# Performance work log

Hardware: AMD Instinct MI355X
Metric: run time of the kernel (lower is better)

## Reference

```python
import jax, jax.numpy as jnp
import numpy as np

TIMESTEPS = 1000
DIFFUSION_SPEED = 0.01
B, N = 4, 2048
E = N * (N - 1) // 2  # strict lower-triangular entries per graph


def _build_Qt():
    # Qt[t-1] = [[1-f, f], [f, 1-f]],  f = 0.5*(1-(1-2s)^t), t = 1..T
    ts = jnp.arange(1, TIMESTEPS + 1, dtype=jnp.float32)
    flip = 0.5 * (1.0 - (1.0 - 2.0 * DIFFUSION_SPEED) ** ts)          # [T]
    row0 = jnp.stack([1.0 - flip, flip], axis=-1)                      # [T,2]
    row1 = jnp.stack([flip, 1.0 - flip], axis=-1)                      # [T,2]
    return jnp.stack([row0, row1], axis=1)                             # [T,2,2]


def setup_inputs() -> dict:
    key = jax.random.key(0)
    k1, k2, k3, k4 = jax.random.split(key, 4)
    adj_start = jax.random.randint(k1, (B, N, N), 0, 2, dtype=jnp.int32)
    t = jax.random.randint(k2, (B,), 0, TIMESTEPS, dtype=jnp.int32)
    u = jax.random.uniform(k3, (B, N, N), dtype=jnp.float32)
    q_approx = jax.random.normal(k4, (B, E), dtype=jnp.float32)
    return {"adj_start": adj_start, "t": t, "u": u, "q_approx": q_approx}


def reference(adj_start, t, u, q_approx):
    Qt = _build_Qt()                                                   # [T,2,2]
    # symmetrize raw adjacency into a binary undirected adjacency
    a = jnp.tril(adj_start, -1)
    adj0 = a + jnp.swapaxes(a, -1, -2)                                 # [B,N,N] in {0,1}

    b_idx = jnp.arange(B)[:, None, None]

    # ---- forward diffusion: sample x_t ~ Categorical(Qt[t][adj0]) ----
    probs = Qt[t][b_idx, adj0]                                         # [B,N,N,2]
    x_t = (u < probs[..., 1]).astype(adj0.dtype)                       # [B,N,N]

    # ---- backward diffusion: q(x_{t-1} | x_t, x_0) ----
    Q_likelihood = Qt[0]                                               # [2,2]
    Q_prior = Qt[t - 1]                                                # [B,2,2] (t=0 wraps, as in torch)
    Q_evidence = Qt[t]                                                 # [B,2,2]

    likelihood = Q_likelihood[x_t]                                     # [B,N,N,2]
    prior = Q_prior[b_idx, adj0]                                       # [B,N,N,2]
    evidence = Q_evidence[b_idx, adj0, x_t]                            # [B,N,N]
    q_backward = likelihood * prior / evidence[..., None]              # [B,N,N,2]

    ti, tj = np.tril_indices(N, -1)                                    # static indices
    q_target = q_backward[:, ti, tj, 1]                                # [B,E]

    # ---- BCE-with-logits loss (mean) ----
    x = q_approx
    loss = jnp.mean(jnp.maximum(x, 0.0) - x * q_target + jnp.log1p(jnp.exp(-jnp.abs(x))))
    return loss
```

## Files before the change

kernel.cpp:

```cpp
#include <hip/hip_runtime.h>
#include <math.h>

#define TIMESTEPS 1000
constexpr int Bc = 4;
constexpr int Nc = 2048;
constexpr int EcI = Nc * (Nc - 1) / 2;
constexpr int EG  = EcI / 4;

constexpr int BLOCKS_PER_B = 512;
constexpr int THREADS      = 256;
constexpr int GSTRIDE      = BLOCKS_PER_B * THREADS;

typedef int   i4v __attribute__((ext_vector_type(4)));
typedef float f4v __attribute__((ext_vector_type(4)));

__device__ __forceinline__ i4v load_i4u(const int* p) {
    i4v r; __builtin_memcpy(&r, p, 16); return r;
}
__device__ __forceinline__ f4v load_f4u(const float* p) {
    f4v r; __builtin_memcpy(&r, p, 16); return r;
}

__global__ __launch_bounds__(256) void diff_loss_kernel(
    const int* __restrict__ adj, const int* __restrict__ t,
    const float* __restrict__ u, const float* __restrict__ q,
    double* __restrict__ partials)
{
    const int b  = blockIdx.x >> 9;
    const int lb = blockIdx.x & (BLOCKS_PER_B - 1);
    const int tb = t[b];

    const float f_t   = 0.5f * (1.0f - powf(0.98f, (float)(tb + 1)));
    const int   tpe   = (tb == 0) ? TIMESTEPS : tb;
    const float f_p   = 0.5f * (1.0f - powf(0.98f, (float)tpe));
    const float f0    = 0.5f * (1.0f - 0.98f);
    const float omf_t = 1.0f - f_t;

    const float p0   = f_t;
    const float p1   = omf_t;
    const float qt00 = f0          * f_p          / omf_t;
    const float qt01 = (1.0f - f0) * f_p          / f_t;
    const float qt10 = f0          * (1.0f - f_p) / f_t;
    const float qt11 = (1.0f - f0) * (1.0f - f_p) / omf_t;

    const int*   adjb = adj + ((size_t)b << 22);
    const float* ub   = u   + ((size_t)b << 22);
    const float* qb   = q   + (size_t)b * EcI;

    double acc = 0.0;
    int g = lb * THREADS + threadIdx.x;

    #pragma unroll 2
    for (int it = 0; it < 4; ++it, g += GSTRIDE) {
        if (g < EG) {
            const int e0 = g << 2;

            const float sf = sqrtf((float)(8 * e0 + 1));
            int i = (int)((1.0f + sf) * 0.5f);
            if (i * (i - 1) / 2 > e0)  --i;
            if (i * (i + 1) / 2 <= e0) ++i;
            const int j = e0 - i * (i - 1) / 2;

            const f4v q4 = *(const f4v*)(qb + e0);
            float s = 0.0f;

            if (j + 4 <= i) {
                const int base = (i << 11) + j;
                const i4v av = load_i4u(adjb + base);
                const f4v uv = load_f4u(ub   + base);
                #pragma unroll
                for (int k = 0; k < 4; ++k) {
                    const int   a0 = av[k];
                    const float ps = a0 ? p1 : p0;
                    const bool  x  = (uv[k] < ps);
                    const float t0 = x ? qt01 : qt00;
                    const float t1 = x ? qt11 : qt10;
                    const float qtv = a0 ? t1 : t0;
                    const float qv  = q4[k];
                    s += fmaxf(qv, 0.0f) - qv * qtv
                       + __logf(1.0f + __expf(-fabsf(qv)));
                }
            } else {
                int ii = i, jj = j;
                #pragma unroll
                for (int k = 0; k < 4; ++k) {
                    const bool adv = (jj >= ii);
                    ii += adv;
                    jj = adv ? 0 : jj;
                    const int base = (ii << 11) + jj;
                    const int   a0 = adjb[base];
                    const float uu = ub[base];
                    const float ps = a0 ? p1 : p0;
                    const bool  x  = (uu < ps);
                    const float t0 = x ? qt01 : qt00;
                    const float t1 = x ? qt11 : qt10;
                    const float qtv = a0 ? t1 : t0;
                    const float qv  = q4[k];
                    s += fmaxf(qv, 0.0f) - qv * qtv
                       + __logf(1.0f + __expf(-fabsf(qv)));
                    ++jj;
                }
            }
            acc += (double)s;
        }
    }

    for (int off = 32; off > 0; off >>= 1)
        acc += __shfl_down(acc, off, 64);
    __shared__ double wsum[4];
    const int lane = threadIdx.x & 63, wid = threadIdx.x >> 6;
    if (lane == 0) wsum[wid] = acc;
    __syncthreads();
    if (threadIdx.x == 0)
        partials[blockIdx.x] = wsum[0] + wsum[1] + wsum[2] + wsum[3];
}

__global__ __launch_bounds__(256) void final_reduce_kernel(
    const double* __restrict__ partials, int nb, float* __restrict__ out)
{
    double acc = 0.0;
    for (int idx = threadIdx.x; idx < nb; idx += blockDim.x)
        acc += partials[idx];
    for (int off = 32; off > 0; off >>= 1)
        acc += __shfl_down(acc, off, 64);
    __shared__ double wsum[4];
    const int lane = threadIdx.x & 63, wid = threadIdx.x >> 6;
    if (lane == 0) wsum[wid] = acc;
    __syncthreads();
    if (threadIdx.x == 0)
        out[0] = (float)((wsum[0] + wsum[1] + wsum[2] + wsum[3]) /
                         ((double)Bc * (double)EcI));
}

extern "C" void kernel_launch(void* const* d_in, const int* in_sizes, int n_in,
                              void* d_out, int out_size, void* d_ws, size_t ws_size,
                              hipStream_t stream) {
    const int*   adj = (const int*)d_in[0];
    const int*   t   = (const int*)d_in[1];
    const float* u   = (const float*)d_in[2];
    const float* q   = (const float*)d_in[3];
    float*  out      = (float*)d_out;
    double* partials = (double*)d_ws;

    const int NB = Bc * BLOCKS_PER_B;
    diff_loss_kernel<<<NB, THREADS, 0, stream>>>(adj, t, u, q, partials);
    final_reduce_kernel<<<1, 256, 0, stream>>>(partials, NB, out);
}
```

Before: 164.5 us.

## Pair complementary triangle rows per block to drop per-element index math

Rows p+1 and 2047-p of the lower triangle are paired so each pair covers a fixed-size span. Each block handles two pairs with aligned 16-byte loads of adj and u, using masked 4-wide groups instead of sqrt-based index recovery and a scalar fallback path. The q loads become scalar and unaligned because row offsets are not multiples of 4, and a single thread handles the leftover group. Launch bounds now also request 8 blocks per multiprocessor.

```diff
diff --git a/kernel.cpp b/kernel.cpp
--- a/kernel.cpp
+++ b/kernel.cpp
@@ -2,38 +2,79 @@
 #include <math.h>
 
 #define TIMESTEPS 1000
-constexpr int Bc = 4;
-constexpr int Nc = 2048;
+constexpr int Bc  = 4;
+constexpr int Nc  = 2048;
 constexpr int EcI = Nc * (Nc - 1) / 2;
-constexpr int EG  = EcI / 4;
-
-constexpr int BLOCKS_PER_B = 512;
-constexpr int THREADS      = 256;
-constexpr int GSTRIDE      = BLOCKS_PER_B * THREADS;
+constexpr int THREADS = 256;
+constexpr int NB  = 2048;
 
 typedef int   i4v __attribute__((ext_vector_type(4)));
 typedef float f4v __attribute__((ext_vector_type(4)));
 
-__device__ __forceinline__ i4v load_i4u(const int* p) {
-    i4v r; __builtin_memcpy(&r, p, 16); return r;
-}
-__device__ __forceinline__ f4v load_f4u(const float* p) {
-    f4v r; __builtin_memcpy(&r, p, 16); return r;
+__device__ __forceinline__ int imin(int a, int b) { return a < b ? a : b; }
+
+struct Grp {
+    i4v av; f4v uv;
+    float q0, q1, q2, q3;
+    int jg, len;
+};
+
+__device__ __forceinline__ Grp load_group(
+    const int* __restrict__ adjb, const float* __restrict__ ub,
+    const float* __restrict__ qb, int gg, int la, int lb, int rb, int Ga)
+{
+    Grp g;
+    const bool ina = gg < Ga;
+    const int row  = ina ? la : rb;
+    g.len = ina ? la : lb;
+    g.jg  = (ina ? gg : (gg - Ga)) << 2;
+    const int base = (row << 11) + g.jg;
+    g.av = *(const i4v*)(adjb + base);
+    g.uv = *(const f4v*)(ub + base);
+    const int tri = (row * (row - 1)) >> 1;
+    const int e   = tri + g.jg;
+    g.q0 = qb[imin(e,     EcI - 1)];
+    g.q1 = qb[imin(e + 1, EcI - 1)];
+    g.q2 = qb[imin(e + 2, EcI - 1)];
+    g.q3 = qb[imin(e + 3, EcI - 1)];
+    return g;
 }
 
-__global__ __launch_bounds__(256) void diff_loss_kernel(
+__device__ __forceinline__ float grp_term(const Grp& g,
+    float p0, float p1, float qt00, float qt01, float qt10, float qt11)
+{
+    const float qs[4] = {g.q0, g.q1, g.q2, g.q3};
+    float s = 0.0f;
+    #pragma unroll
+    for (int k = 0; k < 4; ++k) {
+        const int   a0 = g.av[k];
+        const float ps = a0 ? p1 : p0;
+        const bool  x  = g.uv[k] < ps;
+        const float t0 = x ? qt01 : qt00;
+        const float t1 = x ? qt11 : qt10;
+        const float qt = a0 ? t1 : t0;
+        const float qv = qs[k];
+        const float term = fmaxf(qv, 0.0f) - qv * qt
+                         + __logf(1.0f + __expf(-fabsf(qv)));
+        s += (g.jg + k < g.len) ? term : 0.0f;
+    }
+    return s;
+}
+
+__global__ __launch_bounds__(256, 8) void diff_loss_kernel(
     const int* __restrict__ adj, const int* __restrict__ t,
     const float* __restrict__ u, const float* __restrict__ q,
     double* __restrict__ partials)
 {
-    const int b  = blockIdx.x >> 9;
-    const int lb = blockIdx.x & (BLOCKS_PER_B - 1);
-    const int tb = t[b];
+    const int blk = blockIdx.x;
+    const int b   = blk >> 9;
+    const int ip  = blk & 511;
+    const int tb  = t[b];
 
     const float f_t   = 0.5f * (1.0f - powf(0.98f, (float)(tb + 1)));
     const int   tpe   = (tb == 0) ? TIMESTEPS : tb;
     const float f_p   = 0.5f * (1.0f - powf(0.98f, (float)tpe));
-    const float f0    = 0.5f * (1.0f - 0.98f);
+    const float f0    = 0.01f;
     const float omf_t = 1.0f - f_t;
 
     const float p0   = f_t;
@@ -47,61 +88,35 @@
     const float* ub   = u   + ((size_t)b << 22);
     const float* qb   = q   + (size_t)b * EcI;
 
+    const int tid = threadIdx.x;
     double acc = 0.0;
-    int g = lb * THREADS + threadIdx.x;
 
-    #pragma unroll 2
-    for (int it = 0; it < 4; ++it, g += GSTRIDE) {
-        if (g < EG) {
-            const int e0 = g << 2;
+    #pragma unroll
+    for (int pp = 0; pp < 2; ++pp) {
+        const int p  = 2 * ip + pp;
+        const int la = p + 1;
+        const int rb = 2047 - p;
+        const int lb = (p == 1023) ? 0 : rb;
+        const int Ga = (la + 3) >> 2;
 
-            const float sf = sqrtf((float)(8 * e0 + 1));
-            int i = (int)((1.0f + sf) * 0.5f);
-            if (i * (i - 1) / 2 > e0)  --i;
-            if (i * (i + 1) / 2 <= e0) ++i;
-            const int j = e0 - i * (i - 1) / 2;
+        Grp g0 = load_group(adjb, ub, qb, tid,       la, lb, rb, Ga);
+        Grp g1 = load_group(adjb, ub, qb, tid + 256, la, lb, rb, Ga);
+        acc += (double)grp_term(g0, p0, p1, qt00, qt01, qt10, qt11);
+        acc += (double)grp_term(g1, p0, p1, qt00, qt01, qt10, qt11);
+    }
 
-            const f4v q4 = *(const f4v*)(qb + e0);
-            float s = 0.0f;
-
-            if (j + 4 <= i) {
-                const int base = (i << 11) + j;
-                const i4v av = load_i4u(adjb + base);
-                const f4v uv = load_f4u(ub   + base);
-                #pragma unroll
-                for (int k = 0; k < 4; ++k) {
-                    const int   a0 = av[k];
-                    const float ps = a0 ? p1 : p0;
-                    const bool  x  = (uv[k] < ps);
-                    const float t0 = x ? qt01 : qt00;
-                    const float t1 = x ? qt11 : qt10;
-                    const float qtv = a0 ? t1 : t0;
-                    const float qv  = q4[k];
-                    s += fmaxf(qv, 0.0f) - qv * qtv
-                       + __logf(1.0f + __expf(-fabsf(qv)));
-                }
-            } else {
-                int ii = i, jj = j;
-                #pragma unroll
-                for (int k = 0; k < 4; ++k) {
-                    const bool adv = (jj >= ii);
-                    ii += adv;
-                    jj = adv ? 0 : jj;
-                    const int base = (ii << 11) + jj;
-                    const int   a0 = adjb[base];
-                    const float uu = ub[base];
-                    const float ps = a0 ? p1 : p0;
-                    const bool  x  = (uu < ps);
-                    const float t0 = x ? qt01 : qt00;
-                    const float t1 = x ? qt11 : qt10;
-                    const float qtv = a0 ? t1 : t0;
-                    const float qv  = q4[k];
-                    s += fmaxf(qv, 0.0f) - qv * qtv
-                       + __logf(1.0f + __expf(-fabsf(qv)));
-                    ++jj;
-                }
+    if (tid == 0) {
+        #pragma unroll
+        for (int pp = 0; pp < 2; ++pp) {
+            const int p  = 2 * ip + pp;
+            const int la = p + 1;
+            if (la & 3) {
+                const int rb = 2047 - p;
+                const int lb = (p == 1023) ? 0 : rb;
+                const int Ga = (la + 3) >> 2;
+                Grp gt = load_group(adjb, ub, qb, 512, la, lb, rb, Ga);
+                acc += (double)grp_term(gt, p0, p1, qt00, qt01, qt10, qt11);
             }
-            acc += (double)s;
         }
     }
 
@@ -142,7 +157,6 @@
     float*  out      = (float*)d_out;
     double* partials = (double*)d_ws;
 
-    const int NB = Bc * BLOCKS_PER_B;
     diff_loss_kernel<<<NB, THREADS, 0, stream>>>(adj, t, u, q, partials);
     final_reduce_kernel<<<1, 256, 0, stream>>>(partials, NB, out);
 }
```

Result: no change. 163.3 us (-0.7%).

## Software-pipeline group loads with two-deep prefetch over fewer larger blocks

Applied to the files above, without the earlier changes.

Restructures the main kernel so each thread handles two element groups per iteration, issuing the loads for the groups two iterations ahead while reducing the current ones. The grid shrinks to 128 blocks per graph with a 2D launch, and each thread now covers 16 groups. The vectorized fast path for row-contained groups is dropped in favor of always using scalar per-element gather loads. This aims to hide memory latency via register prefetching, but it raises register pressure and loses the 16-byte vector loads.

```diff
diff --git a/kernel.cpp b/kernel.cpp
--- a/kernel.cpp
+++ b/kernel.cpp
@@ -2,38 +2,80 @@
 #include <math.h>
 
 #define TIMESTEPS 1000
-constexpr int Bc = 4;
-constexpr int Nc = 2048;
+constexpr int Bc  = 4;
+constexpr int Nc  = 2048;
 constexpr int EcI = Nc * (Nc - 1) / 2;
 constexpr int EG  = EcI / 4;
 
-constexpr int BLOCKS_PER_B = 512;
-constexpr int THREADS      = 256;
-constexpr int GSTRIDE      = BLOCKS_PER_B * THREADS;
+constexpr int BLKX    = 128;
+constexpr int THREADS = 256;
+constexpr int ITERS   = 8;
+constexpr int ITERSTRIDE = BLKX * THREADS * 2;
 
 typedef int   i4v __attribute__((ext_vector_type(4)));
 typedef float f4v __attribute__((ext_vector_type(4)));
 
-__device__ __forceinline__ i4v load_i4u(const int* p) {
-    i4v r; __builtin_memcpy(&r, p, 16); return r;
-}
-__device__ __forceinline__ f4v load_f4u(const float* p) {
-    f4v r; __builtin_memcpy(&r, p, 16); return r;
+__device__ __forceinline__ int imin(int a, int b) { return a < b ? a : b; }
+
+struct GData { i4v av; f4v uv; f4v qv; };
+
+__device__ __forceinline__ GData issue_group(
+    const int* __restrict__ adjb, const float* __restrict__ ub,
+    const float* __restrict__ qb, int gc)
+{
+    GData d;
+    const int e0 = gc << 2;
+    const float sf = sqrtf((float)(8 * e0 + 1));
+    int i = (int)((1.0f + sf) * 0.5f);
+    if (i * (i - 1) / 2 > e0)  --i;
+    if (i * (i + 1) / 2 <= e0) ++i;
+    int jj = e0 - i * (i - 1) / 2;
+    d.qv = *(const f4v*)(qb + e0);
+    int ii = i;
+    #pragma unroll
+    for (int k = 0; k < 4; ++k) {
+        const bool adv = (jj >= ii);
+        ii += adv;
+        jj = adv ? 0 : jj;
+        const int base = (ii << 11) + jj;
+        d.av[k] = adjb[base];
+        d.uv[k] = ub[base];
+        ++jj;
+    }
+    return d;
 }
 
-__global__ __launch_bounds__(256) void diff_loss_kernel(
+__device__ __forceinline__ float group_sum(const GData& d,
+    float p0, float p1, float qt00, float qt01, float qt10, float qt11)
+{
+    float s = 0.0f;
+    #pragma unroll
+    for (int k = 0; k < 4; ++k) {
+        const int   a0 = d.av[k];
+        const float ps = a0 ? p1 : p0;
+        const bool  x  = d.uv[k] < ps;
+        const float t0 = x ? qt01 : qt00;
+        const float t1 = x ? qt11 : qt10;
+        const float qt = a0 ? t1 : t0;
+        const float qq = d.qv[k];
+        s += fmaxf(qq, 0.0f) - qq * qt + __logf(1.0f + __expf(-fabsf(qq)));
+    }
+    return s;
+}
+
+__global__ __launch_bounds__(256, 2) void diff_loss_kernel(
     const int* __restrict__ adj, const int* __restrict__ t,
     const float* __restrict__ u, const float* __restrict__ q,
     double* __restrict__ partials)
 {
-    const int b  = blockIdx.x >> 9;
-    const int lb = blockIdx.x & (BLOCKS_PER_B - 1);
+    const int b  = blockIdx.y;
+    const int bx = blockIdx.x;
     const int tb = t[b];
 
     const float f_t   = 0.5f * (1.0f - powf(0.98f, (float)(tb + 1)));
     const int   tpe   = (tb == 0) ? TIMESTEPS : tb;
     const float f_p   = 0.5f * (1.0f - powf(0.98f, (float)tpe));
-    const float f0    = 0.5f * (1.0f - 0.98f);
+    const float f0    = 0.01f;
     const float omf_t = 1.0f - f_t;
 
     const float p0   = f_t;
@@ -47,62 +89,30 @@
     const float* ub   = u   + ((size_t)b << 22);
     const float* qb   = q   + (size_t)b * EcI;
 
+    const int gbase = bx * 512 + threadIdx.x;
+
+    GData A0 = issue_group(adjb, ub, qb, gbase);
+    GData B0 = issue_group(adjb, ub, qb, gbase + 256);
+    GData A1 = issue_group(adjb, ub, qb, gbase + ITERSTRIDE);
+    GData B1 = issue_group(adjb, ub, qb, gbase + ITERSTRIDE + 256);
+
     double acc = 0.0;
-    int g = lb * THREADS + threadIdx.x;
 
-    #pragma unroll 2
-    for (int it = 0; it < 4; ++it, g += GSTRIDE) {
-        if (g < EG) {
-            const int e0 = g << 2;
+    #pragma unroll 1
+    for (int k = 0; k < ITERS; ++k) {
+        GData An = A1, Bn = B1;
+        if (k + 2 < ITERS) {
+            const int gk = gbase + (k + 2) * ITERSTRIDE;
+            An = issue_group(adjb, ub, qb, gk);
+            Bn = issue_group(adjb, ub, qb, imin(gk + 256, EG - 1));
+        }
 
-            const float sf = sqrtf((float)(8 * e0 + 1));
-            int i = (int)((1.0f + sf) * 0.5f);
-            if (i * (i - 1) / 2 > e0)  --i;
-            if (i * (i + 1) / 2 <= e0) ++i;
-            const int j = e0 - i * (i - 1) / 2;
+        const float sA = group_sum(A0, p0, p1, qt00, qt01, qt10, qt11);
+        const float sB = group_sum(B0, p0, p1, qt00, qt01, qt10, qt11);
+        const int g1 = gbase + k * ITERSTRIDE + 256;
+        acc += (double)(sA + ((g1 < EG) ? sB : 0.0f));
 
-            const f4v q4 = *(const f4v*)(qb + e0);
-            float s = 0.0f;
-
-            if (j + 4 <= i) {
-                const int base = (i << 11) + j;
-                const i4v av = load_i4u(adjb + base);
-                const f4v uv = load_f4u(ub   + base);
-                #pragma unroll
-                for (int k = 0; k < 4; ++k) {
-                    const int   a0 = av[k];
-                    const float ps = a0 ? p1 : p0;
-                    const bool  x  = (uv[k] < ps);
-                    const float t0 = x ? qt01 : qt00;
-                    const float t1 = x ? qt11 : qt10;
-                    const float qtv = a0 ? t1 : t0;
-                    const float qv  = q4[k];
-                    s += fmaxf(qv, 0.0f) - qv * qtv
-                       + __logf(1.0f + __expf(-fabsf(qv)));
-                }
-            } else {
-                int ii = i, jj = j;
-                #pragma unroll
-                for (int k = 0; k < 4; ++k) {
-                    const bool adv = (jj >= ii);
-                    ii += adv;
-                    jj = adv ? 0 : jj;
-                    const int base = (ii << 11) + jj;
-                    const int   a0 = adjb[base];
-                    const float uu = ub[base];
-                    const float ps = a0 ? p1 : p0;
-                    const bool  x  = (uu < ps);
-                    const float t0 = x ? qt01 : qt00;
-                    const float t1 = x ? qt11 : qt10;
-                    const float qtv = a0 ? t1 : t0;
-                    const float qv  = q4[k];
-                    s += fmaxf(qv, 0.0f) - qv * qtv
-                       + __logf(1.0f + __expf(-fabsf(qv)));
-                    ++jj;
-                }
-            }
-            acc += (double)s;
-        }
+        A0 = A1; B0 = B1; A1 = An; B1 = Bn;
     }
 
     for (int off = 32; off > 0; off >>= 1)
@@ -112,7 +122,8 @@
     if (lane == 0) wsum[wid] = acc;
     __syncthreads();
     if (threadIdx.x == 0)
-        partials[blockIdx.x] = wsum[0] + wsum[1] + wsum[2] + wsum[3];
+        partials[blockIdx.y * BLKX + blockIdx.x] =
+            wsum[0] + wsum[1] + wsum[2] + wsum[3];
 }
 
 __global__ __launch_bounds__(256) void final_reduce_kernel(
@@ -142,7 +153,7 @@
     float*  out      = (float*)d_out;
     double* partials = (double*)d_ws;
 
-    const int NB = Bc * BLOCKS_PER_B;
-    diff_loss_kernel<<<NB, THREADS, 0, stream>>>(adj, t, u, q, partials);
-    final_reduce_kernel<<<1, 256, 0, stream>>>(partials, NB, out);
+    dim3 grid(BLKX, Bc);
+    diff_loss_kernel<<<grid, THREADS, 0, stream>>>(adj, t, u, q, partials);
+    final_reduce_kernel<<<1, 256, 0, stream>>>(partials, BLKX * Bc, out);
 }
```

Result: no change. 164.8 us (+0.1%).
